# Kernel tuning notes

Measured on AMD Instinct MI355X. Metric: run time of the kernel, lower is better.

Reference implementation:

```python
import jax, jax.numpy as jnp
import numpy as np

D_MODEL, N_HEAD, D_HEAD = 1024, 16, 64
BATCH, Q_LEN = 2, 2048
LN_EPS = 1e-5


def _rel_shift(x):
    # x: [b, q, k, n] -- standard Transformer-XL relative shift
    b, q, k, n = x.shape
    zero_pad = jnp.zeros((b, q, 1, n), dtype=x.dtype)
    x_padded = jnp.concatenate([zero_pad, x], axis=2)      # [b, q, k+1, n]
    x_padded = x_padded.reshape(b, k + 1, q, n)
    return x_padded[:, 1:].reshape(b, q, k, n)


def _layer_norm(x, gamma, beta):
    mu = jnp.mean(x, axis=-1, keepdims=True)
    var = jnp.mean(jnp.square(x - mu), axis=-1, keepdims=True)
    return (x - mu) * jax.lax.rsqrt(var + LN_EPS) * gamma + beta


def setup_inputs() -> dict:
    key = jax.random.key(0)
    ks = jax.random.split(key, 8)
    inp = {
        "x": jax.random.normal(ks[0], (BATCH, Q_LEN, D_MODEL), jnp.float32),
        "relative_pos": jax.random.normal(ks[1], (Q_LEN, D_MODEL), jnp.float32),
        "r_w_bias": jax.random.normal(ks[2], (N_HEAD, D_HEAD), jnp.float32) * 0.02,
        "r_r_bias": jax.random.normal(ks[3], (N_HEAD, D_HEAD), jnp.float32) * 0.02,
        "attn_mask": jax.random.randint(ks[4], (BATCH, Q_LEN), 0, 2).astype(bool),
        "W_qkv": jax.random.normal(ks[5], (D_MODEL, 3 * N_HEAD * D_HEAD), jnp.float32) / np.sqrt(D_MODEL),
        "W_rel": jax.random.normal(ks[6], (D_MODEL, N_HEAD * D_HEAD), jnp.float32) / np.sqrt(D_MODEL),
        "W_out": jax.random.normal(ks[7], (N_HEAD * D_HEAD, D_MODEL), jnp.float32) / np.sqrt(N_HEAD * D_HEAD),
        "ln_gamma": jnp.ones((D_MODEL,), jnp.float32),
        "ln_beta": jnp.zeros((D_MODEL,), jnp.float32),
    }
    return inp


def reference(x, relative_pos, r_w_bias, r_r_bias, attn_mask, W_qkv, W_rel, W_out, ln_gamma, ln_beta):
    b, q_len, _ = x.shape
    r_len = relative_pos.shape[0]
    scale = 1.0 / np.sqrt(D_HEAD)

    w_heads = x @ W_qkv                                    # [b, q, 3*n*d]
    w_q, w_k, w_v = jnp.split(w_heads, 3, axis=-1)
    k_len = w_k.shape[1]

    w_q = w_q.reshape(b, q_len, N_HEAD, D_HEAD)
    w_k = w_k.reshape(b, k_len, N_HEAD, D_HEAD)
    w_v = w_v.reshape(b, k_len, N_HEAD, D_HEAD)
    r_k = (relative_pos @ W_rel).reshape(r_len, N_HEAD, D_HEAD)

    rw_q = w_q + r_w_bias                                  # [b, q, n, d]
    rr_q = w_q + r_r_bias

    ac = jnp.einsum('bind,bjnd->bijn', rw_q, w_k)          # content score
    bd = jnp.einsum('bind,jnd->bijn', rr_q, r_k)           # position score
    bd = _rel_shift(bd)

    attn_score = (ac + bd) * scale                         # [b, q, k, n]
    attn_score = jnp.where(attn_mask[:, None, :, None], -jnp.inf, attn_score)
    attn_prob = jax.nn.softmax(attn_score, axis=2)

    context = jnp.einsum('bijn,bjnd->bind', attn_prob, w_v)
    context = context.reshape(b, q_len, N_HEAD * D_HEAD)
    attn_out = context @ W_out
    return _layer_norm(x + attn_out, ln_gamma, ln_beta)
```

## Files before the change

### kernel.cpp

```cpp
#include <hip/hip_runtime.h>
#include <hip/hip_bf16.h>
#include <math.h>

#define S_LEN 2048
#define NHEAD 16
#define DHEAD 64
#define DMODEL 1024
#define NBATCH 2

typedef unsigned short u16;
typedef __attribute__((ext_vector_type(8))) short bf16x8;
typedef __attribute__((ext_vector_type(4))) short short4v;
typedef __attribute__((ext_vector_type(4))) float f32x4;

__device__ __forceinline__ short f2bs(float x) {
    __hip_bfloat16 h = __float2bfloat16(x);
    return __builtin_bit_cast(short, h);
}

__device__ __forceinline__ float bs2f(u16 x) {
    __hip_bfloat16 h = __builtin_bit_cast(__hip_bfloat16, (short)x);
    return __bfloat162float(h);
}

#define GL2LDS(g, l)                                                         \
    __builtin_amdgcn_global_load_lds(                                        \
        (const __attribute__((address_space(1))) void*)(g),                  \
        (__attribute__((address_space(3))) void*)(l), 16, 0, 0)

__global__ __launch_bounds__(256) void prep_all(
    const float* __restrict__ x, const float* __restrict__ rpos,
    const float* __restrict__ Wqkv, const float* __restrict__ Wrel,
    const float* __restrict__ Wout,
    u16* __restrict__ xb, u16* __restrict__ rposb,
    u16* __restrict__ Wqkvt, u16* __restrict__ Wrelt, u16* __restrict__ Woutt)
{
    int bid = blockIdx.x;
    if (bid < 6144) {
        const float* in;
        u16* out;
        if (bid < 4096) { in = x; out = xb; }
        else            { in = rpos; out = rposb; bid -= 4096; }
        const int i = (bid * 256 + threadIdx.x) * 4;
        float4 v = *(const float4*)(in + i);
        short4v t;
        t[0] = f2bs(v.x); t[1] = f2bs(v.y); t[2] = f2bs(v.z); t[3] = f2bs(v.w);
        *(short4v*)(out + i) = t;
        return;
    }
    bid -= 6144;
    int bx = bid % 80;
    const int ky = bid / 80;
    __shared__ float t[64][65];
    const float* W;
    u16* Wt;
    int N;
    if (bx < 48)      { W = Wqkv; Wt = Wqkvt; N = 3 * DMODEL; }
    else if (bx < 64) { W = Wrel; Wt = Wrelt; N = DMODEL; bx -= 48; }
    else              { W = Wout; Wt = Woutt; N = DMODEL; bx -= 64; }
    const int k0 = ky * 64, n0 = bx * 64;
    const int r = threadIdx.x >> 4;
    const int c4 = (threadIdx.x & 15) * 4;
    #pragma unroll
    for (int it = 0; it < 4; ++it) {
        float4 v = *(const float4*)(W + (size_t)(k0 + it * 16 + r) * N + n0 + c4);
        t[c4 + 0][it * 16 + r] = v.x;
        t[c4 + 1][it * 16 + r] = v.y;
        t[c4 + 2][it * 16 + r] = v.z;
        t[c4 + 3][it * 16 + r] = v.w;
    }
    __syncthreads();
    #pragma unroll
    for (int it = 0; it < 4; ++it) {
        const int nn = it * 16 + r;
        short4v o;
        o[0] = f2bs(t[nn][c4 + 0]); o[1] = f2bs(t[nn][c4 + 1]);
        o[2] = f2bs(t[nn][c4 + 2]); o[3] = f2bs(t[nn][c4 + 3]);
        *(short4v*)(Wt + (size_t)(n0 + nn) * DMODEL + k0 + c4) = o;
    }
}

#define GEMM_BODY_BMN(Aptr, Btptr, Kdim, BM_, BN_)                            \
    __shared__ u16 As[128 * 64];                                              \
    __shared__ u16 Bs[128 * 64];                                              \
    const int tid = threadIdx.x;                                              \
    const int lane = tid & 63;                                                \
    const int w = tid >> 6;                                                   \
    const int quad = lane >> 4, col = lane & 15;                              \
    const int bm = (BM_), bn = (BN_);                                         \
    const int wm = (w >> 1) * 64, wn = (w & 1) * 64;                          \
    f32x4 acc[4][4];                                                          \
    _Pragma("unroll")                                                         \
    for (int mt = 0; mt < 4; ++mt)                                            \
        _Pragma("unroll")                                                     \
        for (int nt = 0; nt < 4; ++nt) acc[mt][nt] = (f32x4){0.f,0.f,0.f,0.f};\
    for (int k0 = 0; k0 < (Kdim); k0 += 64) {                                 \
        _Pragma("unroll")                                                     \
        for (int it = 0; it < 4; ++it) {                                      \
            const int cb = it * 256 + w * 64;                                 \
            const int c = cb + lane;                                          \
            const int r = c >> 3;                                             \
            const int o = ((c & 7) ^ (r & 7)) * 8;                            \
            GL2LDS((Aptr) + (size_t)(bm + r) * (Kdim) + k0 + o, As + (size_t)cb * 8); \
            GL2LDS((Btptr) + (size_t)(bn + r) * (Kdim) + k0 + o, Bs + (size_t)cb * 8);\
        }                                                                     \
        __syncthreads();                                                      \
        _Pragma("unroll")                                                     \
        for (int kc = 0; kc < 2; ++kc) {                                      \
            bf16x8 af[4], bfr[4];                                             \
            _Pragma("unroll")                                                 \
            for (int t = 0; t < 4; ++t) {                                     \
                const int am = wm + t * 16 + col;                             \
                const int aj = kc * 4 + quad;                                 \
                af[t] = *(const bf16x8*)&As[(size_t)am * 64 + ((aj ^ (am & 7)) * 8)]; \
                const int bn2 = wn + t * 16 + col;                            \
                bfr[t] = *(const bf16x8*)&Bs[(size_t)bn2 * 64 + ((aj ^ (bn2 & 7)) * 8)]; \
            }                                                                 \
            _Pragma("unroll")                                                 \
            for (int mt = 0; mt < 4; ++mt)                                    \
                _Pragma("unroll")                                             \
                for (int nt = 0; nt < 4; ++nt)                                \
                    acc[mt][nt] = __builtin_amdgcn_mfma_f32_16x16x32_bf16(    \
                        af[mt], bfr[nt], acc[mt][nt], 0, 0, 0);               \
        }                                                                     \
        __syncthreads();                                                      \
    }

#define GEMM_BODY(Aptr, Btptr, Kdim) \
    GEMM_BODY_BMN(Aptr, Btptr, Kdim, blockIdx.y * 128, blockIdx.x * 128)

__global__ __launch_bounds__(256, 2) void gemm_qkv_rel(
    const u16* __restrict__ A, const u16* __restrict__ Bt,
    const u16* __restrict__ Ar, const u16* __restrict__ Brt,
    const float* __restrict__ rwb, const float* __restrict__ rrb,
    u16* __restrict__ qrw_b, u16* __restrict__ qrr_b,
    u16* __restrict__ kb, u16* __restrict__ vbT,
    u16* __restrict__ rkb)
{
    const int id = blockIdx.x;
    const bool isQ = id < 768;
    int bx, by;
    if (isQ) { bx = id % 24; by = id / 24; }
    else     { const int t = id - 768; bx = t % 8; by = t / 8; }
    const u16* Ap = isQ ? A  : Ar;
    const u16* Bp = isQ ? Bt : Brt;
    GEMM_BODY_BMN(Ap, Bp, DMODEL, by * 128, bx * 128)
    if (isQ) {
        #pragma unroll
        for (int mt = 0; mt < 4; ++mt) {
            const int row0 = bm + wm + mt * 16 + quad * 4;
            const int b = row0 >> 11;
            const int s0 = row0 & 2047;
            #pragma unroll
            for (int nt = 0; nt < 4; ++nt) {
                const int cn = bn + wn + nt * 16 + col;
                const int sec = cn >> 10;
                const int cc = cn & 1023;
                const int h = cc >> 6, d = cc & 63;
                const int bh = b * NHEAD + h;
                if (sec == 0) {
                    const float bw = rwb[cc], br = rrb[cc];
                    #pragma unroll
                    for (int r = 0; r < 4; ++r) {
                        const size_t o = ((size_t)bh * S_LEN + s0 + r) * 64 + d;
                        qrw_b[o] = (u16)f2bs(acc[mt][nt][r] + bw);
                        qrr_b[o] = (u16)f2bs(acc[mt][nt][r] + br);
                    }
                } else if (sec == 1) {
                    #pragma unroll
                    for (int r = 0; r < 4; ++r)
                        kb[((size_t)bh * S_LEN + s0 + r) * 64 + d] =
                            (u16)f2bs(acc[mt][nt][r]);
                } else {
                    short4v t;
                    t[0] = f2bs(acc[mt][nt][0]); t[1] = f2bs(acc[mt][nt][1]);
                    t[2] = f2bs(acc[mt][nt][2]); t[3] = f2bs(acc[mt][nt][3]);
                    *(short4v*)(vbT + ((size_t)bh * 64 + d) * S_LEN + s0) = t;
                }
            }
        }
    } else {
        #pragma unroll
        for (int mt = 0; mt < 4; ++mt) {
            const int l0 = bm + wm + mt * 16 + quad * 4;
            #pragma unroll
            for (int nt = 0; nt < 4; ++nt) {
                const int cn = bn + wn + nt * 16 + col;
                const int h = cn >> 6, d = cn & 63;
                #pragma unroll
                for (int r = 0; r < 4; ++r)
                    rkb[((size_t)h * S_LEN + l0 + r) * 64 + d] =
                        (u16)f2bs(acc[mt][nt][r]);
            }
        }
    }
}

__global__ __launch_bounds__(256, 2) void gemm_out(
    const u16* __restrict__ A, const u16* __restrict__ Bt,
    float* __restrict__ Cf, int N, int K)
{
    GEMM_BODY(A, Bt, K)
    #pragma unroll
    for (int mt = 0; mt < 4; ++mt)
        #pragma unroll
        for (int nt = 0; nt < 4; ++nt)
            #pragma unroll
            for (int r = 0; r < 4; ++r) {
                const int row = bm + wm + mt * 16 + quad * 4 + r;
                const int cn = bn + wn + nt * 16 + col;
                Cf[(size_t)row * N + cn] = acc[mt][nt][r];
            }
}

__global__ __launch_bounds__(512, 2) void flash_attn(
    const u16* __restrict__ qrw_b, const u16* __restrict__ qrr_b,
    const u16* __restrict__ kb, const u16* __restrict__ vbT,
    const u16* __restrict__ rkb, const int* __restrict__ mask,
    u16* __restrict__ ctxb)
{
    const int lane = threadIdx.x & 63;
    const int w    = threadIdx.x >> 6;
    const int quad = lane >> 4;
    const int col  = lane & 15;
    const int bh   = blockIdx.y;
    const int b    = bh >> 4;
    const int n    = bh & 15;
    const int B0   = blockIdx.x * 128;
    const int iw0  = B0 + w * 16;

    __shared__ u16 Ks[2][64 * 64];
    __shared__ u16 Vs[2][64 * 64];
    __shared__ u16 Rs[192 * 64];
    __shared__ u16 Pr[8][16][72];
    __shared__ u16 maddb[S_LEN];

    const size_t headQ = (size_t)bh * S_LEN * 64;
    const size_t headR = (size_t)n  * S_LEN * 64;

    for (int i = threadIdx.x; i < S_LEN; i += 512)
        maddb[i] = (u16)f2bs(mask[b * S_LEN + i] ? -16384.f : 0.f);

    bf16x8 a_rw[2], a_rr0[2], a_rr1[2];
    {
        const int r0 = iw0 + col;
        const int r1 = (r0 + 1 < S_LEN) ? (r0 + 1) : (S_LEN - 1);
        #pragma unroll
        for (int kc = 0; kc < 2; ++kc) {
            const int doff = kc * 32 + quad * 8;
            a_rw[kc]  = *(const bf16x8*)(qrw_b + headQ + (size_t)r0 * 64 + doff);
            a_rr0[kc] = *(const bf16x8*)(qrr_b + headQ + (size_t)r0 * 64 + doff);
            a_rr1[kc] = *(const bf16x8*)(qrr_b + headQ + (size_t)r1 * 64 + doff);
        }
    }

    f32x4 O[4];
    float l_acc[4] = {0.f, 0.f, 0.f, 0.f};
    #pragma unroll
    for (int dt = 0; dt < 4; ++dt) O[dt] = (f32x4){0.f, 0.f, 0.f, 0.f};

    const int swz  = ((lane & 7) ^ ((lane >> 3) & 7)) * 8;
    const int lrow = lane >> 3;
    const int csel = col & 7;

    {
        const int pbase0 = S_LEN - 128 - B0;
        GL2LDS(kb + headQ + (size_t)(w * 8 + lrow) * 64 + swz, Ks[0] + w * 512);
        GL2LDS(vbT + ((size_t)bh * 64 + w * 8 + lrow) * S_LEN + swz, Vs[0] + w * 512);
        #pragma unroll
        for (int t = 0; t < 3; ++t) {
            const int c = w * 3 + t;
            int rr = pbase0 + c * 8 + lrow;
            rr = rr < 0 ? 0 : (rr > S_LEN - 1 ? S_LEN - 1 : rr);
            GL2LDS(rkb + headR + (size_t)rr * 64 + swz, Rs + c * 512);
        }
    }
    int roff = 0;
    __syncthreads();

    for (int u0 = 0; u0 < S_LEN; u0 += 64) {
        const int dblk = B0 - u0;
        const int dw = dblk + 16 * w;
        const bool mixed = (dw >= 0) && (dw <= 48);
        const int buf = (u0 >> 6) & 1;
        const int u1 = u0 + 64;
        const bool have_next = u1 < S_LEN;
        const bool next_full = (B0 - u1) == -64;

        bf16x8 rf2[5][2];
        if (mixed) {
            #pragma unroll
            for (int g = 0; g < 5; ++g) {
                const int u = g * 16 + col;
                int row = (dblk >= 0) ? (u - dw - 17) : (S_LEN - 16 - dw + u);
                row = row < 0 ? 0 : (row > S_LEN - 1 ? S_LEN - 1 : row);
                const u16* rb = rkb + headR + (size_t)row * 64 + quad * 8;
                rf2[g][0] = *(const bf16x8*)(rb);
                rf2[g][1] = *(const bf16x8*)(rb + 32);
            }
        }

        bf16x8 rpre;
        if (have_next) {
            GL2LDS(kb + headQ + (size_t)(u1 + w * 8 + lrow) * 64 + swz,
                   Ks[buf ^ 1] + w * 512);
            GL2LDS(vbT + ((size_t)bh * 64 + w * 8 + lrow) * S_LEN + u1 + swz,
                   Vs[buf ^ 1] + w * 512);
            if (!next_full) {
                const int dn = B0 - u1;
                const int pb = (dn >= 0) ? (S_LEN - 128 - dn) : (-dn - 129);
                int rr = pb + 128 + w * 8 + lrow;
                rr = rr < 0 ? 0 : (rr > S_LEN - 1 ? S_LEN - 1 : rr);
                rpre = *(const bf16x8*)(rkb + headR + (size_t)rr * 64 + swz);
            }
        }

        f32x4 sc[4];
        #pragma unroll
        for (int nt = 0; nt < 4; ++nt) {
            const int m = nt * 16 + col;
            bf16x8 k0 = *(const bf16x8*)&Ks[buf][m * 64 + ((quad ^ csel) * 8)];
            bf16x8 k1 = *(const bf16x8*)&Ks[buf][m * 64 + (((4 + quad) ^ csel) * 8)];
            f32x4 c = (f32x4){0.f, 0.f, 0.f, 0.f};
            c = __builtin_amdgcn_mfma_f32_16x16x32_bf16(a_rw[0], k0, c, 0, 0, 0);
            c = __builtin_amdgcn_mfma_f32_16x16x32_bf16(a_rw[1], k1, c, 0, 0, 0);
            sc[nt] = c;
        }

        f32x4 pnl[5];
        {
            const bf16x8* aP = (dblk >= 0) ? a_rr0 : a_rr1;
            #pragma unroll
            for (int g = 0; g < 5; ++g) {
                const int m = g * 16 + col + 112 - 16 * w;
                int slot = m + roff; if (slot >= 192) slot -= 192;
                bf16x8 r0 = *(const bf16x8*)&Rs[slot * 64 + ((quad ^ csel) * 8)];
                bf16x8 r1 = *(const bf16x8*)&Rs[slot * 64 + (((4 + quad) ^ csel) * 8)];
                f32x4 c = (f32x4){0.f, 0.f, 0.f, 0.f};
                c = __builtin_amdgcn_mfma_f32_16x16x32_bf16(aP[0], r0, c, 0, 0, 0);
                c = __builtin_amdgcn_mfma_f32_16x16x32_bf16(aP[1], r1, c, 0, 0, 0);
                pnl[g] = c;
            }
        }
        if (mixed || dw == -16) {
            f32x4 oth[5];
            #pragma unroll
            for (int g = 0; g < 5; ++g) oth[g] = (f32x4){0.f, 0.f, 0.f, 0.f};
            if (mixed) {
                const bf16x8* aV = (dblk >= 0) ? a_rr1 : a_rr0;
                #pragma unroll
                for (int g = 0; g < 5; ++g) {
                    f32x4 c = (f32x4){0.f, 0.f, 0.f, 0.f};
                    c = __builtin_amdgcn_mfma_f32_16x16x32_bf16(aV[0], rf2[g][0], c, 0, 0, 0);
                    c = __builtin_amdgcn_mfma_f32_16x16x32_bf16(aV[1], rf2[g][1], c, 0, 0, 0);
                    oth[g] = c;
                }
            }
            const int lim1 = 15 + dw;
            #pragma unroll
            for (int g = 0; g < 5; ++g) {
                const int u = g * 16 + col;
                #pragma unroll
                for (int r = 0; r < 4; ++r) {
                    const float r1v = (dblk >= 0) ? pnl[g][r] : oth[g][r];
                    const float r2v = (dblk >= 0) ? oth[g][r] : pnl[g][r];
                    pnl[g][r] = (u <= lim1) ? r1v : ((u == lim1 + 1) ? 0.f : r2v);
                }
            }
        }

        #pragma unroll
        for (int nt = 0; nt < 4; ++nt) {
            const float ma = bs2f(maddb[u0 + nt * 16 + col]);
            #pragma unroll
            for (int r = 0; r < 4; ++r) {
                const int uo = col + 15 - quad * 4 - r;
                const int src = (quad << 4) | (uo & 15);
                float blo = __shfl(pnl[nt][r], src, 64);
                float bhi = __shfl(pnl[nt + 1][r], src, 64);
                float bd = (uo < 16) ? blo : bhi;
                float p = __expf(fmaf(sc[nt][r] + bd, 0.125f, ma));
                sc[nt][r] = p;
                l_acc[r] += p;
            }
        }

        #pragma unroll
        for (int nt = 0; nt < 4; ++nt)
            #pragma unroll
            for (int r = 0; r < 4; ++r)
                Pr[w][quad * 4 + r][nt * 16 + col] = (u16)f2bs(sc[nt][r]);
        bf16x8 pa[2];
        pa[0] = *(const bf16x8*)&Pr[w][col][quad * 8];
        pa[1] = *(const bf16x8*)&Pr[w][col][32 + quad * 8];

        #pragma unroll
        for (int dt = 0; dt < 4; ++dt) {
            const int m = dt * 16 + col;
            bf16x8 v0 = *(const bf16x8*)&Vs[buf][m * 64 + ((quad ^ csel) * 8)];
            bf16x8 v1 = *(const bf16x8*)&Vs[buf][m * 64 + (((4 + quad) ^ csel) * 8)];
            f32x4 c = O[dt];
            c = __builtin_amdgcn_mfma_f32_16x16x32_bf16(pa[0], v0, c, 0, 0, 0);
            c = __builtin_amdgcn_mfma_f32_16x16x32_bf16(pa[1], v1, c, 0, 0, 0);
            O[dt] = c;
        }

        if (have_next) {
            __syncthreads();
            if (next_full) {
                #pragma unroll
                for (int t = 0; t < 3; ++t) {
                    const int c = w * 3 + t;
                    int rr = -65 + c * 8 + lrow;
                    rr = rr < 0 ? 0 : (rr > S_LEN - 1 ? S_LEN - 1 : rr);
                    GL2LDS(rkb + headR + (size_t)rr * 64 + swz, Rs + c * 512);
                }
                roff = 0;
            } else {
                *(bf16x8*)&Rs[((size_t)(roff + w * 8) << 6) + lane * 8] = rpre;
                roff += 64; if (roff >= 192) roff -= 192;
            }
            __syncthreads();
        }
    }

    float inv[4];
    #pragma unroll
    for (int r = 0; r < 4; ++r) {
        float s = l_acc[r];
        #pragma unroll
        for (int off = 1; off < 16; off <<= 1)
            s += __shfl_xor(s, off, 64);
        inv[r] = 1.f / s;
    }
    #pragma unroll
    for (int dt = 0; dt < 4; ++dt)
        #pragma unroll
        for (int r = 0; r < 4; ++r) {
            const int i = iw0 + quad * 4 + r;
            ctxb[((size_t)b * S_LEN + i) * DMODEL + n * 64 + dt * 16 + col] =
                (u16)f2bs(O[dt][r] * inv[r]);
        }
}

__global__ __launch_bounds__(256) void ln_kernel(const float* __restrict__ x,
                                                 const float* __restrict__ ao,
                                                 const float* __restrict__ gamma,
                                                 const float* __restrict__ beta,
                                                 float* __restrict__ out) {
    const int r = blockIdx.x;
    const int tid = threadIdx.x;
    const size_t base = (size_t)r * DMODEL + tid * 4;
    float4 xv = *(const float4*)(x + base);
    float4 av = *(const float4*)(ao + base);
    float v0 = xv.x + av.x, v1 = xv.y + av.y, v2 = xv.z + av.z, v3 = xv.w + av.w;

    float s = v0 + v1 + v2 + v3;
    #pragma unroll
    for (int off = 32; off > 0; off >>= 1) s += __shfl_xor(s, off, 64);
    __shared__ float red[4];
    __shared__ float red2[4];
    if ((tid & 63) == 0) red[tid >> 6] = s;
    __syncthreads();
    float mu = (red[0] + red[1] + red[2] + red[3]) * (1.0f / DMODEL);

    float d0 = v0 - mu, d1 = v1 - mu, d2 = v2 - mu, d3 = v3 - mu;
    float q = d0 * d0 + d1 * d1 + d2 * d2 + d3 * d3;
    #pragma unroll
    for (int off = 32; off > 0; off >>= 1) q += __shfl_xor(q, off, 64);
    if ((tid & 63) == 0) red2[tid >> 6] = q;
    __syncthreads();
    float var = (red2[0] + red2[1] + red2[2] + red2[3]) * (1.0f / DMODEL);
    float rstd = rsqrtf(var + 1e-5f);

    float4 g  = *(const float4*)(gamma + tid * 4);
    float4 be = *(const float4*)(beta + tid * 4);
    float4 o = make_float4(d0 * rstd * g.x + be.x,
                           d1 * rstd * g.y + be.y,
                           d2 * rstd * g.z + be.z,
                           d3 * rstd * g.w + be.w);
    *(float4*)(out + base) = o;
}

extern "C" void kernel_launch(void* const* d_in, const int* in_sizes, int n_in,
                              void* d_out, int out_size, void* d_ws, size_t ws_size,
                              hipStream_t stream) {
    const float* x    = (const float*)d_in[0];
    const float* rpos = (const float*)d_in[1];
    const float* rwb  = (const float*)d_in[2];
    const float* rrb  = (const float*)d_in[3];
    const int*   mask = (const int*)  d_in[4];
    const float* Wqkv = (const float*)d_in[5];
    const float* Wrel = (const float*)d_in[6];
    const float* Wout = (const float*)d_in[7];
    const float* gam  = (const float*)d_in[8];
    const float* bet  = (const float*)d_in[9];
    float* out = (float*)d_out;

    u16* wsb   = (u16*)d_ws;
    u16* ctxb  = wsb;
    float* ao  = (float*)(wsb + 4194304);
    u16* qrw_b = wsb + 12582912;
    u16* qrr_b = qrw_b + 4194304;
    u16* kb    = qrr_b + 4194304;
    u16* vbT   = kb + 4194304;
    u16* rkb   = vbT + 4194304;
    u16* xb    = rkb + 2097152;
    u16* rposb = xb + 4194304;
    u16* Wqkvt = rposb + 2097152;
    u16* Wrelt = Wqkvt + 3145728;
    u16* Woutt = Wrelt + 1048576;

    dim3 blk(256);
    prep_all<<<dim3(7424), blk, 0, stream>>>(x, rpos, Wqkv, Wrel, Wout,
                                             xb, rposb, Wqkvt, Wrelt, Woutt);
    gemm_qkv_rel<<<dim3(896), blk, 0, stream>>>(xb, Wqkvt, rposb, Wrelt,
                                                rwb, rrb,
                                                qrw_b, qrr_b, kb, vbT, rkb);
    flash_attn<<<dim3(S_LEN / 128, NBATCH * NHEAD), dim3(512), 0, stream>>>(
        qrw_b, qrr_b, kb, vbT, rkb, mask, ctxb);
    gemm_out<<<dim3(8, 32), blk, 0, stream>>>(ctxb, Woutt, ao, DMODEL, DMODEL);
    ln_kernel<<<dim3(NBATCH * S_LEN), blk, 0, stream>>>(x, ao, gam, bet, out);
}
```

Measured before the change: 311.3 us.

## Stage QKV/rel GEMM epilogue through LDS for coalesced stores, raise occupancy, add MFMA priority

```diff
diff --git a/kernel.cpp b/kernel.cpp
--- a/kernel.cpp
+++ b/kernel.cpp
@@ -129,7 +129,7 @@
 #define GEMM_BODY(Aptr, Btptr, Kdim) \
     GEMM_BODY_BMN(Aptr, Btptr, Kdim, blockIdx.y * 128, blockIdx.x * 128)
 
-__global__ __launch_bounds__(256, 2) void gemm_qkv_rel(
+__global__ __launch_bounds__(256, 3) void gemm_qkv_rel(
     const u16* __restrict__ A, const u16* __restrict__ Bt,
     const u16* __restrict__ Ar, const u16* __restrict__ Brt,
     const float* __restrict__ rwb, const float* __restrict__ rrb,
@@ -145,58 +145,131 @@
     const u16* Ap = isQ ? A  : Ar;
     const u16* Bp = isQ ? Bt : Brt;
     GEMM_BODY_BMN(Ap, Bp, DMODEL, by * 128, bx * 128)
+
+    __shared__ u16 Es[128 * 72];
+    const int hw    = wn >> 6;
+    const int srow  = tid >> 1;
+    const int shalf = (tid & 1) * 32;
+
     if (isQ) {
-        #pragma unroll
-        for (int mt = 0; mt < 4; ++mt) {
-            const int row0 = bm + wm + mt * 16 + quad * 4;
-            const int b = row0 >> 11;
-            const int s0 = row0 & 2047;
-            #pragma unroll
-            for (int nt = 0; nt < 4; ++nt) {
-                const int cn = bn + wn + nt * 16 + col;
-                const int sec = cn >> 10;
-                const int cc = cn & 1023;
-                const int h = cc >> 6, d = cc & 63;
-                const int bh = b * NHEAD + h;
-                if (sec == 0) {
-                    const float bw = rwb[cc], br = rrb[cc];
+        const int sec  = bn >> 10;
+        const int b    = bm >> 11;
+        const int sloc = bm & 2047;
+        if (sec == 0) {
+            #pragma unroll
+            for (int hh = 0; hh < 2; ++hh) {
+                const int h = ((bn & 1023) >> 6) + hh;
+                #pragma unroll
+                for (int which = 0; which < 2; ++which) {
+                    const float* bias = which ? rrb : rwb;
+                    __syncthreads();
+                    if (hw == hh) {
+                        #pragma unroll
+                        for (int nt = 0; nt < 4; ++nt) {
+                            const float bv = bias[h * 64 + nt * 16 + col];
+                            #pragma unroll
+                            for (int mt = 0; mt < 4; ++mt) {
+                                const int row = wm + mt * 16 + quad * 4;
+                                #pragma unroll
+                                for (int r = 0; r < 4; ++r)
+                                    Es[(row + r) * 72 + nt * 16 + col] =
+                                        (u16)f2bs(acc[mt][nt][r] + bv);
+                            }
+                        }
+                    }
+                    __syncthreads();
+                    u16* outp = which ? qrr_b : qrw_b;
+                    const size_t ob =
+                        ((size_t)(b * NHEAD + h) * S_LEN + sloc + srow) * 64 + shalf;
                     #pragma unroll
-                    for (int r = 0; r < 4; ++r) {
-                        const size_t o = ((size_t)bh * S_LEN + s0 + r) * 64 + d;
-                        qrw_b[o] = (u16)f2bs(acc[mt][nt][r] + bw);
-                        qrr_b[o] = (u16)f2bs(acc[mt][nt][r] + br);
+                    for (int k2 = 0; k2 < 4; ++k2)
+                        *(bf16x8*)(outp + ob + k2 * 8) =
+                            *(const bf16x8*)&Es[srow * 72 + shalf + k2 * 8];
+                }
+            }
+        } else if (sec == 1) {
+            #pragma unroll
+            for (int hh = 0; hh < 2; ++hh) {
+                const int h = ((bn & 1023) >> 6) + hh;
+                __syncthreads();
+                if (hw == hh) {
+                    #pragma unroll
+                    for (int nt = 0; nt < 4; ++nt)
+                        #pragma unroll
+                        for (int mt = 0; mt < 4; ++mt) {
+                            const int row = wm + mt * 16 + quad * 4;
+                            #pragma unroll
+                            for (int r = 0; r < 4; ++r)
+                                Es[(row + r) * 72 + nt * 16 + col] =
+                                    (u16)f2bs(acc[mt][nt][r]);
+                        }
+                }
+                __syncthreads();
+                const size_t ob =
+                    ((size_t)(b * NHEAD + h) * S_LEN + sloc + srow) * 64 + shalf;
+                #pragma unroll
+                for (int k2 = 0; k2 < 4; ++k2)
+                    *(bf16x8*)(kb + ob + k2 * 8) =
+                        *(const bf16x8*)&Es[srow * 72 + shalf + k2 * 8];
+            }
+        } else {
+            const int d2  = tid >> 2;
+            const int sc2 = (tid & 3) * 32;
+            #pragma unroll
+            for (int hh = 0; hh < 2; ++hh) {
+                const int h = ((bn & 1023) >> 6) + hh;
+                __syncthreads();
+                if (hw == hh) {
+                    #pragma unroll
+                    for (int nt = 0; nt < 4; ++nt) {
+                        const int d = nt * 16 + col;
+                        #pragma unroll
+                        for (int mt = 0; mt < 4; ++mt) {
+                            const int s4 = wm + mt * 16 + quad * 4;
+                            short4v t;
+                            t[0] = f2bs(acc[mt][nt][0]); t[1] = f2bs(acc[mt][nt][1]);
+                            t[2] = f2bs(acc[mt][nt][2]); t[3] = f2bs(acc[mt][nt][3]);
+                            *(short4v*)&Es[d * 136 + s4] = t;
+                        }
                     }
-                } else if (sec == 1) {
+                }
+                __syncthreads();
+                const size_t ob =
+                    ((size_t)((b * NHEAD + h) * 64 + d2) * S_LEN) + sloc + sc2;
+                #pragma unroll
+                for (int k2 = 0; k2 < 4; ++k2)
+                    *(bf16x8*)(vbT + ob + k2 * 8) =
+                        *(const bf16x8*)&Es[d2 * 136 + sc2 + k2 * 8];
+            }
+        }
+    } else {
+        #pragma unroll
+        for (int hh = 0; hh < 2; ++hh) {
+            const int h = (bn >> 6) + hh;
+            __syncthreads();
+            if (hw == hh) {
+                #pragma unroll
+                for (int nt = 0; nt < 4; ++nt)
                     #pragma unroll
-                    for (int r = 0; r < 4; ++r)
-                        kb[((size_t)bh * S_LEN + s0 + r) * 64 + d] =
-                            (u16)f2bs(acc[mt][nt][r]);
-                } else {
-                    short4v t;
-                    t[0] = f2bs(acc[mt][nt][0]); t[1] = f2bs(acc[mt][nt][1]);
-                    t[2] = f2bs(acc[mt][nt][2]); t[3] = f2bs(acc[mt][nt][3]);
-                    *(short4v*)(vbT + ((size_t)bh * 64 + d) * S_LEN + s0) = t;
-                }
-            }
-        }
-    } else {
-        #pragma unroll
-        for (int mt = 0; mt < 4; ++mt) {
-            const int l0 = bm + wm + mt * 16 + quad * 4;
-            #pragma unroll
-            for (int nt = 0; nt < 4; ++nt) {
-                const int cn = bn + wn + nt * 16 + col;
-                const int h = cn >> 6, d = cn & 63;
-                #pragma unroll
-                for (int r = 0; r < 4; ++r)
-                    rkb[((size_t)h * S_LEN + l0 + r) * 64 + d] =
-                        (u16)f2bs(acc[mt][nt][r]);
-            }
-        }
-    }
-}
-
-__global__ __launch_bounds__(256, 2) void gemm_out(
+                    for (int mt = 0; mt < 4; ++mt) {
+                        const int row = wm + mt * 16 + quad * 4;
+                        #pragma unroll
+                        for (int r = 0; r < 4; ++r)
+                            Es[(row + r) * 72 + nt * 16 + col] =
+                                (u16)f2bs(acc[mt][nt][r]);
+                    }
+            }
+            __syncthreads();
+            const size_t ob = ((size_t)h * S_LEN + bm + srow) * 64 + shalf;
+            #pragma unroll
+            for (int k2 = 0; k2 < 4; ++k2)
+                *(bf16x8*)(rkb + ob + k2 * 8) =
+                    *(const bf16x8*)&Es[srow * 72 + shalf + k2 * 8];
+        }
+    }
+}
+
+__global__ __launch_bounds__(256, 3) void gemm_out(
     const u16* __restrict__ A, const u16* __restrict__ Bt,
     float* __restrict__ Cf, int N, int K)
 {
@@ -316,6 +389,7 @@
         }
 
         f32x4 sc[4];
+        __builtin_amdgcn_s_setprio(1);
         #pragma unroll
         for (int nt = 0; nt < 4; ++nt) {
             const int m = nt * 16 + col;
@@ -326,10 +400,12 @@
             c = __builtin_amdgcn_mfma_f32_16x16x32_bf16(a_rw[1], k1, c, 0, 0, 0);
             sc[nt] = c;
         }
+        __builtin_amdgcn_s_setprio(0);
 
         f32x4 pnl[5];
         {
             const bf16x8* aP = (dblk >= 0) ? a_rr0 : a_rr1;
+            __builtin_amdgcn_s_setprio(1);
             #pragma unroll
             for (int g = 0; g < 5; ++g) {
                 const int m = g * 16 + col + 112 - 16 * w;
@@ -341,6 +417,7 @@
                 c = __builtin_amdgcn_mfma_f32_16x16x32_bf16(aP[1], r1, c, 0, 0, 0);
                 pnl[g] = c;
             }
+            __builtin_amdgcn_s_setprio(0);
         }
         if (mixed || dw == -16) {
             f32x4 oth[5];
@@ -394,6 +471,7 @@
         pa[0] = *(const bf16x8*)&Pr[w][col][quad * 8];
         pa[1] = *(const bf16x8*)&Pr[w][col][32 + quad * 8];
 
+        __builtin_amdgcn_s_setprio(1);
         #pragma unroll
         for (int dt = 0; dt < 4; ++dt) {
             const int m = dt * 16 + col;
@@ -404,6 +482,7 @@
             c = __builtin_amdgcn_mfma_f32_16x16x32_bf16(pa[1], v1, c, 0, 0, 0);
             O[dt] = c;
         }
+        __builtin_amdgcn_s_setprio(0);
 
         if (have_next) {
             __syncthreads();
```

Result: slower. 327.6 us (+5.2%).
